# Kernel tuning notes

Measured on AMD Instinct MI355X. Metric: run time of the kernel, lower is better.

## Reference

```python
import jax, jax.numpy as jnp
import numpy as np

NF, IN_NF, N_LAYERS = 64, 196, 3
B, H, W = 1, 256, 256
P3 = [(1, 1), (1, 1)]
P1 = [(0, 0), (0, 0)]


def conv2d(x, w, pad):
    return jax.lax.conv_general_dilated(x, w, (1, 1), pad,
                                        dimension_numbers=('NCHW', 'OIHW', 'NCHW'))


def prelu(x, a):
    return jnp.where(x >= 0, x, a[None, :, None, None] * x)


def warp(x, flow):
    # standard backward bilinear warp, zero padding outside the image
    Bx, C, Hx, Wx = x.shape
    yy, xx = jnp.meshgrid(jnp.arange(Hx, dtype=x.dtype),
                          jnp.arange(Wx, dtype=x.dtype), indexing='ij')
    px = xx[None] + flow[:, 0]  # (B,H,W)
    py = yy[None] + flow[:, 1]

    def sample(img, px, py):  # img (C,H,W); px,py (H,W)
        x0 = jnp.floor(px)
        y0 = jnp.floor(py)
        x1 = x0 + 1.0
        y1 = y0 + 1.0
        wx1 = px - x0
        wx0 = 1.0 - wx1
        wy1 = py - y0
        wy0 = 1.0 - wy1

        def gather(xi, yi):
            valid = (xi >= 0) & (xi <= Wx - 1) & (yi >= 0) & (yi <= Hx - 1)
            xc = jnp.clip(xi, 0, Wx - 1).astype(jnp.int32)
            yc = jnp.clip(yi, 0, Hx - 1).astype(jnp.int32)
            return img[:, yc, xc] * valid.astype(img.dtype)

        return (gather(x0, y0) * (wx0 * wy0) + gather(x1, y0) * (wx1 * wy0)
                + gather(x0, y1) * (wx0 * wy1) + gather(x1, y1) * (wx1 * wy1))

    return jax.vmap(sample)(x, px, py)


def setup_inputs() -> dict:
    key = jax.random.key(0)
    ks = jax.random.split(key, 11)
    s = 0.05
    return {
        'feat_0': jax.random.normal(ks[0], (B, 64, H, W), jnp.float32),
        'feat_1': jax.random.normal(ks[1], (B, 64, H, W), jnp.float32),
        'feat_dense': jax.random.normal(ks[2], (B, 64, H, W), jnp.float32),
        'flow': jax.random.normal(ks[3], (B, 4, H, W), jnp.float32),
        'space_mask': jax.random.uniform(ks[4], (B, 1, H, W), jnp.float32),
        'head_w': jax.random.normal(ks[5], (IN_NF, IN_NF, 3, 3), jnp.float32) * s,
        'head_a': jnp.full((IN_NF,), 0.25, jnp.float32),
        'conv_w': jax.random.normal(ks[6], (N_LAYERS, IN_NF, IN_NF, 3, 3), jnp.float32) * s,
        'conv_a': jnp.full((N_LAYERS, IN_NF), 0.25, jnp.float32),
        'last_w': jax.random.normal(ks[7], (4 + NF, IN_NF * (N_LAYERS + 1), 1, 1), jnp.float32) * s,
        'last_b': jax.random.normal(ks[8], (4 + NF,), jnp.float32) * s,
        'mask_w': jax.random.normal(ks[9], (2, NF, 3, 3), jnp.float32) * s,
        'mask_b': jax.random.normal(ks[10], (2,), jnp.float32) * s,
    }


def reference(feat_0, feat_1, feat_dense, flow, space_mask,
              head_w, head_a, conv_w, conv_a, last_w, last_b, mask_w, mask_b):
    f0 = warp(feat_0, flow[:, :2])
    f1 = warp(feat_1, flow[:, 2:4])
    x = jnp.concatenate([f0, f1, feat_dense, flow], axis=1)  # (B, in_nf, H, W)
    sm_up = jnp.repeat(jnp.repeat(space_mask, 2, axis=2), 2, axis=3)

    # head: conv3x3 -> PReLU, then mask (dense / use_sparsity=False path)
    x = prelu(conv2d(x, head_w, P3), head_a) * space_mask
    outs = [x]
    for i in range(N_LAYERS):
        x = conv2d(x, conv_w[i], P3) * space_mask
        x = prelu(x, conv_a[i])
        outs.append(x)
    x = conv2d(jnp.concatenate(outs, axis=1), last_w, P1) + last_b[None, :, None, None]

    smn = conv2d(x[:, 4:], mask_w, P3) + mask_b[None, :, None, None]

    Bx, Cx, Hx, Wx = x.shape
    x_up = jax.image.resize(x, (Bx, Cx, 2 * Hx, 2 * Wx), method='bilinear')
    smn_up = jax.image.resize(smn, (Bx, 2, 2 * Hx, 2 * Wx), method='bilinear')

    flow_out = x_up[:, :4]
    feat_t = x_up[:, 4:]
    # eval-mode mask (training=False): hard argmax between channel 0 and 1
    mask_next = (smn_up[:, :1] > smn_up[:, 1:2]).astype(x.dtype) * sm_up
    return flow_out, feat_t, mask_next
```

## Files before the change

### kernel.cpp

```cpp
#include <hip/hip_runtime.h>

typedef _Float16 f16;
typedef _Float16 f16x8 __attribute__((ext_vector_type(8)));
typedef _Float16 f16x4 __attribute__((ext_vector_type(4)));
typedef float    f32x4 __attribute__((ext_vector_type(4)));
typedef float    f32x16 __attribute__((ext_vector_type(16)));

#define MFMA16(a,b,c) __builtin_amdgcn_mfma_f32_16x16x32_f16(a,b,c,0,0,0)
#define MFMA32(a,b,c) __builtin_amdgcn_mfma_f32_32x32x16_f16(a,b,c,0,0,0)

#define NPIX 65536
#define PXS   8
#define KHS   2064
#define K16S  4128
#define HS    8256
#define CBS   16512
#define ROWH  115584
#define RBYTES 231168
#define SBUF  ((size_t)258*RBYTES)

#define PKSUB  7168
#define PKCB   43008
#define PK_CONV 903168

#define PKL_CB  5120
#define PKL_BI  35840

#define BSTG 16640

__global__ void k_pack_conv(const float* __restrict__ head_w,
                            const float* __restrict__ conv_w,
                            f16* __restrict__ dst)
{
    int t = blockIdx.x*256 + threadIdx.x;
    int lane = t & 63; t >>= 6;
    int ob  = t % 7;  t /= 7;
    int sel = t & 1;  t >>= 1;
    int kx  = t % 3;  t /= 3;
    int k16 = t & 1;  t >>= 1;
    int cb  = t % 7;  t /= 7;
    int ky  = t % 3;  t /= 3;
    int li  = t;
    if (li >= 4) return;
    const float* W = (li == 0) ? head_w : (conv_w + (size_t)(li-1)*196*196*9);
    int oc  = ob*32 + (lane & 31);
    int ic0 = cb*32 + k16*16 + (lane >> 5)*8;
    int tap = ky*3 + kx;
    f16x8 v;
#pragma unroll
    for (int j = 0; j < 8; ++j) {
        int ic = ic0 + j;
        float x = 0.f;
        if (oc < 196 && ic < 196) x = W[((size_t)oc*196 + ic)*9 + tap];
        f16 h = (f16)x;
        v[j] = (sel == 0) ? h : (f16)(x - (float)h);
    }
    size_t frag = (((((size_t)(ky*7+cb)*2 + k16)*3 + kx)*2 + sel)*7 + ob);
    *(f16x8*)(dst + (size_t)li*PK_CONV + frag*512 + (size_t)lane*8) = v;
}

__global__ void k_pack_last(const float* __restrict__ last_w, f16* __restrict__ dst)
{
    int t = blockIdx.x*256 + threadIdx.x;
    if (t >= 4*7*5*2*64) return;
    int lane = t & 63; t >>= 6;
    int sel  = t & 1;  t >>= 1;
    int ob   = t % 5;  t /= 5;
    int cb   = t % 7;  t /= 7;
    int bi   = t;
    int oc = ob*16 + (lane & 15);
    int k0 = cb*32 + (lane >> 4)*8;
    f16x8 v;
#pragma unroll
    for (int j = 0; j < 8; ++j) {
        int k = k0 + j;
        float x = 0.f;
        if (oc < 68 && k < 196) x = last_w[(size_t)oc*784 + bi*196 + k];
        f16 h = (f16)x;
        v[j] = (sel == 0) ? h : (f16)(x - (float)h);
    }
    *(f16x8*)(dst + (((size_t)((bi*7+cb)*5 + ob)*2 + sel)*64 + lane)*8) = v;
}

__global__ void k_zero_halo(f16* __restrict__ bufA, f16* __restrict__ bufB)
{
    int c = blockIdx.x*256 + threadIdx.x;
    int end = c & 1; c >>= 1;
    int kh  = c & 1; c >>= 1;
    int k16 = c & 1; c >>= 1;
    int h   = c & 1; c >>= 1;
    int cb  = c % 7; c /= 7;
    int row = c % 258; c /= 258;
    if (c >= 2) return;
    f16* base = (c == 0) ? bufA : bufB;
    f16* p = base + (size_t)row*ROWH + cb*CBS + h*HS + k16*K16S + kh*KHS + (end ? 257 : 0)*PXS;
    f16x8 z = {(f16)0,(f16)0,(f16)0,(f16)0,(f16)0,(f16)0,(f16)0,(f16)0};
    *(f16x8*)p = z;
}

struct Gath { int o00,o01,o10,o11; float w00,w01,w10,w11; };

__device__ inline Gath mk_gath(float pxf, float pyf)
{
    float x0 = floorf(pxf), y0 = floorf(pyf);
    float x1 = x0 + 1.f, y1 = y0 + 1.f;
    float wx1 = pxf - x0, wx0 = 1.f - wx1;
    float wy1 = pyf - y0, wy0 = 1.f - wy1;
    bool vx0 = (x0 >= 0.f) && (x0 <= 255.f);
    bool vx1 = (x1 >= 0.f) && (x1 <= 255.f);
    bool vy0 = (y0 >= 0.f) && (y0 <= 255.f);
    bool vy1 = (y1 >= 0.f) && (y1 <= 255.f);
    int ix0 = min(max((int)x0, 0), 255);
    int ix1 = min(max((int)x1, 0), 255);
    int iy0 = min(max((int)y0, 0), 255);
    int iy1 = min(max((int)y1, 0), 255);
    Gath g;
    g.o00 = iy0*256 + ix0; g.w00 = (vx0 && vy0) ? wx0*wy0 : 0.f;
    g.o01 = iy0*256 + ix1; g.w01 = (vx1 && vy0) ? wx1*wy0 : 0.f;
    g.o10 = iy1*256 + ix0; g.w10 = (vx0 && vy1) ? wx0*wy1 : 0.f;
    g.o11 = iy1*256 + ix1; g.w11 = (vx1 && vy1) ? wx1*wy1 : 0.f;
    return g;
}

__device__ inline void store4n(f16* __restrict__ rowb, int slot, int c0,
                               float a, float b, float c, float d)
{
    f16x4 hi, lo;
    f16 h;
    h = (f16)a; hi[0] = h; lo[0] = (f16)(a - (float)h);
    h = (f16)b; hi[1] = h; lo[1] = (f16)(b - (float)h);
    h = (f16)c; hi[2] = h; lo[2] = (f16)(c - (float)h);
    h = (f16)d; hi[3] = h; lo[3] = (f16)(d - (float)h);
    int cb = c0 >> 5, w32 = c0 & 31;
    f16* p = rowb + cb*CBS + (w32 >> 4)*K16S + ((w32 >> 3) & 1)*KHS
                 + (size_t)slot*PXS + (w32 & 7);
    *(f16x4*)p        = hi;
    *(f16x4*)(p + HS) = lo;
}

__global__ void k_warp_concat(const float* __restrict__ f0, const float* __restrict__ f1,
                              const float* __restrict__ fd, const float* __restrict__ flow,
                              f16* __restrict__ out)
{
    int px = blockIdx.x*256 + threadIdx.x;
    int row = px >> 8, col = px & 255;
    f16* rowb = out + (size_t)(row+1)*ROWH;
    int slot = col + 1;
    Gath g0 = mk_gath((float)col + flow[px],          (float)row + flow[NPIX   + px]);
    Gath g1 = mk_gath((float)col + flow[2*NPIX + px], (float)row + flow[3*NPIX + px]);
#pragma unroll
    for (int c = 0; c < 64; c += 4) {
        float v[4];
#pragma unroll
        for (int r = 0; r < 4; ++r) {
            const float* im = f0 + (size_t)(c+r)*NPIX;
            v[r] = g0.w00*im[g0.o00] + g0.w01*im[g0.o01] + g0.w10*im[g0.o10] + g0.w11*im[g0.o11];
        }
        store4n(rowb, slot, c, v[0], v[1], v[2], v[3]);
    }
#pragma unroll
    for (int c = 0; c < 64; c += 4) {
        float v[4];
#pragma unroll
        for (int r = 0; r < 4; ++r) {
            const float* im = f1 + (size_t)(c+r)*NPIX;
            v[r] = g1.w00*im[g1.o00] + g1.w01*im[g1.o01] + g1.w10*im[g1.o10] + g1.w11*im[g1.o11];
        }
        store4n(rowb, slot, 64 + c, v[0], v[1], v[2], v[3]);
    }
#pragma unroll
    for (int c = 0; c < 64; c += 4) {
        store4n(rowb, slot, 128 + c, fd[(size_t)(c+0)*NPIX + px], fd[(size_t)(c+1)*NPIX + px],
                                     fd[(size_t)(c+2)*NPIX + px], fd[(size_t)(c+3)*NPIX + px]);
    }
    store4n(rowb, slot, 192, flow[px], flow[NPIX+px], flow[2*NPIX+px], flow[3*NPIX+px]);
#pragma unroll
    for (int c = 196; c < 224; c += 4) store4n(rowb, slot, c, 0.f, 0.f, 0.f, 0.f);
}

template<int NOB, int OB0>
__device__ __forceinline__ void sub_step(const f16* __restrict__ ws, const char* __restrict__ bs,
                                         f32x16 (&acc)[4][2])
{
    f16x8 Ah[NOB], Al[NOB];
#pragma unroll
    for (int o = 0; o < NOB; ++o) {
        Ah[o] = *(const f16x8*)(ws + (OB0 + o)*512);
        Al[o] = *(const f16x8*)(ws + 3584 + (OB0 + o)*512);
    }
    f16x8 Bh[2], Bl[2];
    Bh[0] = *(const f16x8*)(bs);
    Bl[0] = *(const f16x8*)(bs + 4*2080);
    Bh[1] = *(const f16x8*)(bs + 512);
    Bl[1] = *(const f16x8*)(bs + 512 + 4*2080);
#pragma unroll
    for (int o = 0; o < NOB; ++o) {
#pragma unroll
        for (int pt = 0; pt < 2; ++pt) {
            acc[o][pt] = MFMA32(Ah[o], Bh[pt], acc[o][pt]);
            acc[o][pt] = MFMA32(Al[o], Bh[pt], acc[o][pt]);
            acc[o][pt] = MFMA32(Ah[o], Bl[pt], acc[o][pt]);
        }
    }
}

__global__ __launch_bounds__(256, 2)
void k_conv32(const f16* __restrict__ in, f16* __restrict__ out,
              const f16* __restrict__ pack, const float* __restrict__ alpha,
              const float* __restrict__ mask)
{
    __shared__ __align__(16) char Bs[2][BSTG];

    int bid = blockIdx.x;
    int wg  = (bid & 7)*64 + (bid >> 3);
    int row  = wg >> 1;
    int half = wg & 1;
    int tid  = threadIdx.x;
    int lane = tid & 63;
    int w    = tid >> 6;
    int ocg  = ((w >> 1) ^ bid) & 1;
    int pxg  = w & 1;
    int l31 = lane & 31, lk = lane >> 5;
    int cb0 = half*128;

    f32x16 acc[4][2];
#pragma unroll
    for (int o = 0; o < 4; ++o)
#pragma unroll
        for (int pt = 0; pt < 2; ++pt)
#pragma unroll
            for (int e = 0; e < 16; ++e) acc[o][pt][e] = 0.f;

    auto stage = [&](int b, const f16* g) {
#pragma unroll
        for (int u = 0; u < 5; ++u) {
            int c = tid + u*256;
            if (u < 4 || c < 1040) {
                int pl = c / 130;
                int i  = c - pl*130;
                const f16* src = g + (size_t)pl*KHS + (size_t)(cb0 + i)*PXS;
                __builtin_amdgcn_global_load_lds(
                    (const __attribute__((address_space(1))) void*)src,
                    (__attribute__((address_space(3))) void*)(&Bs[b][0] + c*16),
                    16, 0, 0);
            }
        }
    };

    const int lbase = lk*2080 + (pxg*64 + l31)*16;

    const f16* g = in + (size_t)row*ROWH;
    stage(0, g);
    __syncthreads();

    int bsel = 0, cbc = 0;
    for (int ph = 0; ph < 21; ++ph) {
        if (ph < 20) {
            if (cbc < 6) { g += CBS; ++cbc; }
            else         { g += ROWH - 6*CBS; cbc = 0; }
            stage(bsel ^ 1, g);
        }
        const f16* wcb = pack + (size_t)ph*PKCB + (size_t)lane*8;
        const char* bl = &Bs[bsel][0] + lbase;
        if (ocg == 0) {
#pragma unroll
            for (int k16 = 0; k16 < 2; ++k16)
#pragma unroll
                for (int kx = 0; kx < 3; ++kx)
                    sub_step<4,0>(wcb + (k16*3+kx)*PKSUB, bl + k16*4160 + kx*16, acc);
        } else {
#pragma unroll
            for (int k16 = 0; k16 < 2; ++k16)
#pragma unroll
                for (int kx = 0; kx < 3; ++kx)
                    sub_step<3,4>(wcb + (k16*3+kx)*PKSUB, bl + k16*4160 + kx*16, acc);
        }
        __syncthreads();
        bsel ^= 1;
    }

    int nob = (ocg == 0) ? 4 : 3;
    int ob0 = (ocg == 0) ? 0 : 4;
    int colbase = cb0 + pxg*64;
    float mv[2];
#pragma unroll
    for (int pt = 0; pt < 2; ++pt) mv[pt] = mask[row*256 + colbase + pt*32 + l31];
#pragma unroll
    for (int o = 0; o < 4; ++o) {
        if (o >= nob) continue;
        int ob = ob0 + o;
#pragma unroll
        for (int qg = 0; qg < 4; ++qg) {
            int oc0 = ob*32 + 8*qg + 4*lk;
            f32x4 a4 = *(const f32x4*)(alpha + min(oc0, 192));
#pragma unroll
            for (int pt = 0; pt < 2; ++pt) {
                f16x4 hi, lo;
#pragma unroll
                for (int e = 0; e < 4; ++e) {
                    float v = acc[o][pt][qg*4 + e];
                    v = (v >= 0.f ? v : a4[e]*v) * mv[pt];
                    f16 h = (f16)v;
                    hi[e] = h;
                    lo[e] = (f16)(v - (float)h);
                }
                f16* p = out + (size_t)(row+1)*ROWH + (size_t)(colbase + pt*32 + l31 + 1)*PXS
                       + lk*4 + ob*CBS + (qg >> 1)*K16S + (qg & 1)*KHS;
                *(f16x4*)p        = hi;
                *(f16x4*)(p + HS) = lo;
            }
        }
    }
}

__global__ __launch_bounds__(256, 4)
void k_acc_last(const f16* __restrict__ in, const f16* __restrict__ pack,
                const float* __restrict__ bias, float* __restrict__ accp, int bi)
{
    int lane = threadIdx.x & 63;
    int wid  = (blockIdx.x << 2) | (threadIdx.x >> 6);
    int row  = wid >> 3;
    int col0 = (wid & 7) << 5;
    int l15 = lane & 15, lk = lane >> 4;

    f32x4 acc[5][2];
#pragma unroll
    for (int i = 0; i < 5; ++i)
#pragma unroll
        for (int j = 0; j < 2; ++j)
            acc[i][j] = (f32x4){0.f, 0.f, 0.f, 0.f};

    const f16* bb = in + (size_t)(row+1)*ROWH + (size_t)(col0 + l15 + 1)*PXS
                  + (lk >> 1)*K16S + (lk & 1)*KHS;
    const f16* ap = pack + (size_t)bi*PKL_BI + (size_t)lane*8;
    for (int cb = 0; cb < 7; ++cb) {
        f16x8 bh[2], bl[2];
#pragma unroll
        for (int pb = 0; pb < 2; ++pb) {
            const f16* p = bb + cb*CBS + pb*16*PXS;
            bh[pb] = *(const f16x8*)p;
            bl[pb] = *(const f16x8*)(p + HS);
        }
        const f16* a = ap + cb*PKL_CB;
#pragma unroll
        for (int ob = 0; ob < 5; ++ob) {
            f16x8 ah = *(const f16x8*)(a + ob*1024);
            f16x8 al = *(const f16x8*)(a + ob*1024 + 512);
#pragma unroll
            for (int pb = 0; pb < 2; ++pb) {
                acc[ob][pb] = MFMA16(ah, bh[pb], acc[ob][pb]);
                acc[ob][pb] = MFMA16(ah, bl[pb], acc[ob][pb]);
                acc[ob][pb] = MFMA16(al, bh[pb], acc[ob][pb]);
            }
        }
    }
#pragma unroll
    for (int ob = 0; ob < 5; ++ob) {
        int oc0 = ob*16 + lk*4;
        if (oc0 >= 72) continue;
#pragma unroll
        for (int pb = 0; pb < 2; ++pb) {
            int px = row*256 + col0 + pb*16 + l15;
            float* dst = accp + (size_t)px*72 + oc0;
            f32x4 d = acc[ob][pb];
            if (bi == 0) {
                f32x4 b4;
#pragma unroll
                for (int r = 0; r < 4; ++r) b4[r] = bias[min(oc0 + r, 67)];
                *(f32x4*)dst = d + b4;
            } else {
                *(f32x4*)dst = *(const f32x4*)dst + d;
            }
        }
    }
}

__global__ void k_smn(const float* __restrict__ accp, const float* __restrict__ mw,
                      const float* __restrict__ mb, float* __restrict__ smn)
{
    int px = blockIdx.x*256 + threadIdx.x;
    int row = px >> 8, col = px & 255;
    float s0 = mb[0], s1 = mb[1];
    for (int ky = 0; ky < 3; ++ky) {
        int r = row + ky - 1;
        if ((unsigned)r > 255u) continue;
        for (int kx = 0; kx < 3; ++kx) {
            int c = col + kx - 1;
            if ((unsigned)c > 255u) continue;
            const float* ab = accp + ((size_t)r*256 + c)*72 + 4;
            const float* w  = mw + ky*3 + kx;
#pragma unroll
            for (int ch = 0; ch < 64; ch += 4) {
                f32x4 v = *(const f32x4*)(ab + ch);
                s0 += v[0]*w[(ch+0)*9] + v[1]*w[(ch+1)*9] + v[2]*w[(ch+2)*9] + v[3]*w[(ch+3)*9];
                s1 += v[0]*w[(64+ch+0)*9] + v[1]*w[(64+ch+1)*9] + v[2]*w[(64+ch+2)*9] + v[3]*w[(64+ch+3)*9];
            }
        }
    }
    smn[px]        = s0;
    smn[NPIX + px] = s1;
}

__global__ void k_upsample(const float* __restrict__ accp, float* __restrict__ outp)
{
    int o = blockIdx.x*256 + threadIdx.x;
    int oy = o >> 9, ox = o & 511;
    int my = oy >> 1, mx = ox >> 1;
    int r0, r1, c0, c1; float wy0, wy1, wx0, wx1;
    if (oy & 1) { r0 = my;            r1 = min(my+1, 255); wy0 = 0.75f; wy1 = 0.25f; }
    else        { r0 = max(my-1, 0);  r1 = my;             wy0 = 0.25f; wy1 = 0.75f; }
    if (ox & 1) { c0 = mx;            c1 = min(mx+1, 255); wx0 = 0.75f; wx1 = 0.25f; }
    else        { c0 = max(mx-1, 0);  c1 = mx;             wx0 = 0.25f; wx1 = 0.75f; }
    const float* p00 = accp + ((size_t)r0*256 + c0)*72;
    const float* p01 = accp + ((size_t)r0*256 + c1)*72;
    const float* p10 = accp + ((size_t)r1*256 + c0)*72;
    const float* p11 = accp + ((size_t)r1*256 + c1)*72;
    float w00 = wy0*wx0, w01 = wy0*wx1, w10 = wy1*wx0, w11 = wy1*wx1;
#pragma unroll
    for (int ch = 0; ch < 68; ch += 4) {
        f32x4 va = *(const f32x4*)(p00 + ch);
        f32x4 vb = *(const f32x4*)(p01 + ch);
        f32x4 vc = *(const f32x4*)(p10 + ch);
        f32x4 vd = *(const f32x4*)(p11 + ch);
        f32x4 v;
#pragma unroll
        for (int r = 0; r < 4; ++r)
            v[r] = w00*va[r] + w01*vb[r] + w10*vc[r] + w11*vd[r];
        outp[(size_t)(ch+0)*262144 + o] = v[0];
        outp[(size_t)(ch+1)*262144 + o] = v[1];
        outp[(size_t)(ch+2)*262144 + o] = v[2];
        outp[(size_t)(ch+3)*262144 + o] = v[3];
    }
}

__global__ void k_mask(const float* __restrict__ smn, const float* __restrict__ sm,
                       float* __restrict__ outp)
{
    int o = blockIdx.x*256 + threadIdx.x;
    int oy = o >> 9, ox = o & 511;
    int my = oy >> 1, mx = ox >> 1;
    int r0, r1, c0, c1; float wy0, wy1, wx0, wx1;
    if (oy & 1) { r0 = my;            r1 = min(my+1, 255); wy0 = 0.75f; wy1 = 0.25f; }
    else        { r0 = max(my-1, 0);  r1 = my;             wy0 = 0.25f; wy1 = 0.75f; }
    if (ox & 1) { c0 = mx;            c1 = min(mx+1, 255); wx0 = 0.75f; wx1 = 0.25f; }
    else        { c0 = max(mx-1, 0);  c1 = mx;             wx0 = 0.25f; wx1 = 0.75f; }
    float w00 = wy0*wx0, w01 = wy0*wx1, w10 = wy1*wx0, w11 = wy1*wx1;
    int i00 = r0*256 + c0, i01 = r0*256 + c1, i10 = r1*256 + c0, i11 = r1*256 + c1;
    float s0 = w00*smn[i00] + w01*smn[i01] + w10*smn[i10] + w11*smn[i11];
    float s1 = w00*smn[NPIX+i00] + w01*smn[NPIX+i01] + w10*smn[NPIX+i10] + w11*smn[NPIX+i11];
    outp[(size_t)68*262144 + o] = (s0 > s1) ? sm[my*256 + mx] : 0.f;
}

extern "C" void kernel_launch(void* const* d_in, const int* in_sizes, int n_in,
                              void* d_out, int out_size, void* d_ws, size_t ws_size,
                              hipStream_t stream)
{
    const float* feat0  = (const float*)d_in[0];
    const float* feat1  = (const float*)d_in[1];
    const float* featd  = (const float*)d_in[2];
    const float* flow   = (const float*)d_in[3];
    const float* smask  = (const float*)d_in[4];
    const float* head_w = (const float*)d_in[5];
    const float* head_a = (const float*)d_in[6];
    const float* conv_w = (const float*)d_in[7];
    const float* conv_a = (const float*)d_in[8];
    const float* last_w = (const float*)d_in[9];
    const float* last_b = (const float*)d_in[10];
    const float* mask_w = (const float*)d_in[11];
    const float* mask_b = (const float*)d_in[12];
    float* outp = (float*)d_out;

    char* ws = (char*)d_ws;
    size_t off = 0;
    f16* bufA = (f16*)(ws + off); off += SBUF;
    f16* bufB = (f16*)(ws + off); off += SBUF;
    f16* packc = (f16*)(ws + off); off += (size_t)4*PK_CONV*2;
    f16* packl = (f16*)(ws + off); off += (size_t)4*PKL_BI*2;
    float* accp = (float*)(ws + off); off += (size_t)NPIX*72*4;
    float* smn  = (float*)(ws + off); off += (size_t)2*NPIX*4;

    hipMemsetAsync(bufA, 0, RBYTES, stream);
    hipMemsetAsync((char*)bufA + (size_t)257*RBYTES, 0, RBYTES, stream);
    hipMemsetAsync(bufB, 0, RBYTES, stream);
    hipMemsetAsync((char*)bufB + (size_t)257*RBYTES, 0, RBYTES, stream);
    k_zero_halo<<<226, 256, 0, stream>>>(bufA, bufB);

    k_pack_conv<<<1764, 256, 0, stream>>>(head_w, conv_w, packc);
    k_pack_last<<<70, 256, 0, stream>>>(last_w, packl);
    k_warp_concat<<<256, 256, 0, stream>>>(feat0, feat1, featd, flow, bufA);

    k_conv32<<<512, 256, 0, stream>>>(bufA, bufB, packc, head_a, smask);
    k_acc_last<<<512, 256, 0, stream>>>(bufB, packl, last_b, accp, 0);
    k_conv32<<<512, 256, 0, stream>>>(bufB, bufA, packc + (size_t)1*PK_CONV, conv_a, smask);
    k_acc_last<<<512, 256, 0, stream>>>(bufA, packl, last_b, accp, 1);
    k_conv32<<<512, 256, 0, stream>>>(bufA, bufB, packc + (size_t)2*PK_CONV, conv_a + 196, smask);
    k_acc_last<<<512, 256, 0, stream>>>(bufB, packl, last_b, accp, 2);
    k_conv32<<<512, 256, 0, stream>>>(bufB, bufA, packc + (size_t)3*PK_CONV, conv_a + 392, smask);
    k_acc_last<<<512, 256, 0, stream>>>(bufA, packl, last_b, accp, 3);

    k_smn<<<256, 256, 0, stream>>>(accp, mask_w, mask_b, smn);
    k_upsample<<<1024, 256, 0, stream>>>(accp, outp);
    k_mask<<<1024, 256, 0, stream>>>(smn, smask, outp);
}
```

Before: 851.5 us.

## Stage conv weight tiles into LDS with double buffering instead of global loads

Weights (A operands) were read straight from global memory by every wave inside the MFMA loop. They are now copied into a double-buffered LDS tile per sub-step with global_load_lds and shared across the waves, while the input tile keeps its existing double buffering. This cuts redundant global/L2 traffic for the weights. In exchange it adds a __syncthreads per sub-step (six per phase instead of one) and more LDS use, which may lower occupancy.

```diff
diff --git a/kernel.cpp b/kernel.cpp
--- a/kernel.cpp
+++ b/kernel.cpp
@@ -26,6 +26,7 @@
 #define PKL_CB  5120
 #define PKL_BI  35840
 
+#define ASTG 14336
 #define BSTG 16640
 
 __global__ void k_pack_conv(const float* __restrict__ head_w,
@@ -179,27 +180,23 @@
 }
 
 template<int NOB, int OB0>
-__device__ __forceinline__ void sub_step(const f16* __restrict__ ws, const char* __restrict__ bs,
-                                         f32x16 (&acc)[4][2])
-{
-    f16x8 Ah[NOB], Al[NOB];
+__device__ __forceinline__ void micro(const char* __restrict__ ab, const char* __restrict__ bl,
+                                      f32x16 (&acc)[4][2], int lane)
+{
+    f16x8 Bh[2], Bl[2];
+    Bh[0] = *(const f16x8*)(bl);
+    Bh[1] = *(const f16x8*)(bl + 512);
+    Bl[0] = *(const f16x8*)(bl + 8320);
+    Bl[1] = *(const f16x8*)(bl + 8320 + 512);
 #pragma unroll
     for (int o = 0; o < NOB; ++o) {
-        Ah[o] = *(const f16x8*)(ws + (OB0 + o)*512);
-        Al[o] = *(const f16x8*)(ws + 3584 + (OB0 + o)*512);
-    }
-    f16x8 Bh[2], Bl[2];
-    Bh[0] = *(const f16x8*)(bs);
-    Bl[0] = *(const f16x8*)(bs + 4*2080);
-    Bh[1] = *(const f16x8*)(bs + 512);
-    Bl[1] = *(const f16x8*)(bs + 512 + 4*2080);
-#pragma unroll
-    for (int o = 0; o < NOB; ++o) {
+        f16x8 Ah = *(const f16x8*)(ab + (OB0 + o)*1024 + lane*16);
+        f16x8 Al = *(const f16x8*)(ab + (7 + OB0 + o)*1024 + lane*16);
 #pragma unroll
         for (int pt = 0; pt < 2; ++pt) {
-            acc[o][pt] = MFMA32(Ah[o], Bh[pt], acc[o][pt]);
-            acc[o][pt] = MFMA32(Al[o], Bh[pt], acc[o][pt]);
-            acc[o][pt] = MFMA32(Ah[o], Bl[pt], acc[o][pt]);
+            acc[o][pt] = MFMA32(Ah, Bh[pt], acc[o][pt]);
+            acc[o][pt] = MFMA32(Al, Bh[pt], acc[o][pt]);
+            acc[o][pt] = MFMA32(Ah, Bl[pt], acc[o][pt]);
         }
     }
 }
@@ -209,6 +206,7 @@
               const f16* __restrict__ pack, const float* __restrict__ alpha,
               const float* __restrict__ mask)
 {
+    __shared__ __align__(16) char As[2][ASTG];
     __shared__ __align__(16) char Bs[2][BSTG];
 
     int bid = blockIdx.x;
@@ -231,7 +229,23 @@
 #pragma unroll
             for (int e = 0; e < 16; ++e) acc[o][pt][e] = 0.f;
 
-    auto stage = [&](int b, const f16* g) {
+    auto stageA = [&](int b, const f16* src) {
+        __builtin_amdgcn_global_load_lds(
+            (const __attribute__((address_space(1))) void*)(src + (size_t)tid*8),
+            (__attribute__((address_space(3))) void*)(&As[b][0] + tid*16), 16, 0, 0);
+        __builtin_amdgcn_global_load_lds(
+            (const __attribute__((address_space(1))) void*)(src + (size_t)(tid+256)*8),
+            (__attribute__((address_space(3))) void*)(&As[b][0] + (tid+256)*16), 16, 0, 0);
+        __builtin_amdgcn_global_load_lds(
+            (const __attribute__((address_space(1))) void*)(src + (size_t)(tid+512)*8),
+            (__attribute__((address_space(3))) void*)(&As[b][0] + (tid+512)*16), 16, 0, 0);
+        if (tid < 128)
+            __builtin_amdgcn_global_load_lds(
+                (const __attribute__((address_space(1))) void*)(src + (size_t)(tid+768)*8),
+                (__attribute__((address_space(3))) void*)(&As[b][0] + (tid+768)*16), 16, 0, 0);
+    };
+
+    auto stageB = [&](int b, const f16* g) {
 #pragma unroll
         for (int u = 0; u < 5; ++u) {
             int c = tid + u*256;
@@ -250,32 +264,27 @@
     const int lbase = lk*2080 + (pxg*64 + l31)*16;
 
     const f16* g = in + (size_t)row*ROWH;
-    stage(0, g);
+    stageB(0, g);
+    stageA(0, pack);
     __syncthreads();
 
-    int bsel = 0, cbc = 0;
+    int asel = 0, bsel = 0, cbc = 0, q = 0;
     for (int ph = 0; ph < 21; ++ph) {
         if (ph < 20) {
             if (cbc < 6) { g += CBS; ++cbc; }
             else         { g += ROWH - 6*CBS; cbc = 0; }
-            stage(bsel ^ 1, g);
-        }
-        const f16* wcb = pack + (size_t)ph*PKCB + (size_t)lane*8;
-        const char* bl = &Bs[bsel][0] + lbase;
-        if (ocg == 0) {
-#pragma unroll
-            for (int k16 = 0; k16 < 2; ++k16)
-#pragma unroll
-                for (int kx = 0; kx < 3; ++kx)
-                    sub_step<4,0>(wcb + (k16*3+kx)*PKSUB, bl + k16*4160 + kx*16, acc);
-        } else {
-#pragma unroll
-            for (int k16 = 0; k16 < 2; ++k16)
-#pragma unroll
-                for (int kx = 0; kx < 3; ++kx)
-                    sub_step<3,4>(wcb + (k16*3+kx)*PKSUB, bl + k16*4160 + kx*16, acc);
-        }
-        __syncthreads();
+            stageB(bsel ^ 1, g);
+        }
+#pragma unroll
+        for (int s = 0; s < 6; ++s) {
+            if (q < 125) stageA(asel ^ 1, pack + (size_t)(q+1)*PKSUB);
+            const char* ab = &As[asel][0];
+            const char* bl = &Bs[bsel][0] + lbase + (s/3)*4160 + (s%3)*16;
+            if (ocg == 0) micro<4,0>(ab, bl, acc, lane);
+            else          micro<3,4>(ab, bl, acc, lane);
+            __syncthreads();
+            asel ^= 1; ++q;
+        }
         bsel ^= 1;
     }
 
```

New measurement: 806.5 us. 5.3% less time.
